# Optimization experiments

Measured on AMD Instinct MI355X. Metric: run time of the kernel, lower is better.

## Reference

```python
import jax, jax.numpy as jnp
import numpy as np

D_MODEL = 1024
D_STATE = 64
HEADDIM = 64
EXPAND = 2
D_INNER = D_MODEL * EXPAND          # 2048
NHEADS = D_INNER // HEADDIM          # 32
D_IN_PROJ = 2 * D_INNER + 2 * D_STATE + NHEADS  # 4256
BATCH, SEQLEN = 4, 4096


def layernorm(x, w, b, eps=1e-5):
    mu = jnp.mean(x, axis=-1, keepdims=True)
    var = jnp.mean(jnp.square(x - mu), axis=-1, keepdims=True)
    return (x - mu) * jax.lax.rsqrt(var + eps) * w + b


def setup_inputs() -> dict:
    key = jax.random.key(0)
    ks = jax.random.split(key, 5)
    x = jax.random.normal(ks[0], (BATCH, SEQLEN, D_MODEL), dtype=jnp.float32)
    # xavier-ish small init (gain 0.5) as in _init_weights
    in_proj_w = jax.random.normal(ks[1], (D_IN_PROJ, D_MODEL), dtype=jnp.float32) * 0.5 * np.sqrt(2.0 / (D_IN_PROJ + D_MODEL))
    out_proj_w = jax.random.normal(ks[2], (D_MODEL, D_INNER), dtype=jnp.float32) * 0.5 * np.sqrt(2.0 / (D_MODEL + D_INNER))
    A_log = jnp.log(jnp.arange(1, NHEADS + 1, dtype=jnp.float32))
    dt_bias = jax.random.normal(ks[3], (NHEADS,), dtype=jnp.float32) * 0.01 + 0.1
    Dparam = jnp.ones((NHEADS,), dtype=jnp.float32)
    return {
        'x': x, 'in_proj_w': in_proj_w, 'out_proj_w': out_proj_w,
        'A_log': A_log, 'dt_bias': dt_bias, 'Dparam': Dparam,
        'ln_w': jnp.ones((D_INNER,), jnp.float32), 'ln_b': jnp.zeros((D_INNER,), jnp.float32),
        'ni_w': jnp.ones((D_MODEL,), jnp.float32), 'ni_b': jnp.zeros((D_MODEL,), jnp.float32),
        'no_w': jnp.ones((D_MODEL,), jnp.float32), 'no_b': jnp.zeros((D_MODEL,), jnp.float32),
    }


def _selective_scan(x_multi, A, Bm, Cm, dt):
    # x_multi: [B,L,H,P], A: [H], Bm/Cm: [B,L,N], dt: [B,L,H]
    Bb, L, H, P = x_multi.shape
    N = Bm.shape[-1]
    dA = jnp.minimum(jnp.exp(dt * A[None, None, :]), 0.99)  # [B,L,H]

    def step(h, inp):
        x_t, B_t, C_t, dA_t = inp  # [B,H,P], [B,N], [B,N], [B,H]
        dBx = jnp.einsum('bhp,bn->bhpn', x_t, B_t)
        h = jnp.clip(dA_t[:, :, None, None] * h + dBx, -10.0, 10.0)
        y_t = jnp.einsum('bn,bhpn->bhp', C_t, h)
        return h, y_t

    h0 = jnp.zeros((Bb, H, P, N), dtype=x_multi.dtype)
    xs = (jnp.moveaxis(x_multi, 1, 0), jnp.moveaxis(Bm, 1, 0),
          jnp.moveaxis(Cm, 1, 0), jnp.moveaxis(dA, 1, 0))
    _, y = jax.lax.scan(step, h0, xs)  # y: [L,B,H,P]
    return jnp.moveaxis(y, 0, 1)


def reference(x, in_proj_w, out_proj_w, A_log, dt_bias, Dparam,
              ln_w, ln_b, ni_w, ni_b, no_w, no_b):
    Bb, L, Dm = x.shape
    x_norm = layernorm(x, ni_w, ni_b)
    zxbcdt = jnp.einsum('bld,ed->ble', x_norm, in_proj_w)  # [B,L,D_IN_PROJ]
    z = zxbcdt[..., :D_INNER]
    x_ssm = zxbcdt[..., D_INNER:2 * D_INNER]
    Bm = zxbcdt[..., 2 * D_INNER:2 * D_INNER + D_STATE]
    Cm = zxbcdt[..., 2 * D_INNER + D_STATE:2 * D_INNER + 2 * D_STATE]
    dt = zxbcdt[..., 2 * D_INNER + 2 * D_STATE:]
    dt = jnp.clip(jax.nn.softplus(dt + dt_bias[None, None, :]), 0.001, 0.1)  # [B,L,H]
    A = -jnp.exp(A_log)  # [H]
    x_multi = x_ssm.reshape(Bb, L, NHEADS, HEADDIM)
    y = _selective_scan(x_multi, A, Bm, Cm, dt)  # [B,L,H,P]
    y = y + x_multi * Dparam[None, None, :, None]  # D skip
    y = y.reshape(Bb, L, D_INNER)
    y = y * jax.nn.silu(z)
    y = layernorm(y, ln_w, ln_b)
    y = jnp.einsum('ble,de->bld', y, out_proj_w)
    y = jnp.clip(y, -10.0, 10.0)
    y = layernorm(y, no_w, no_b)
    return y
```

## Files before the change

kernel.cpp:

```cpp
#include <hip/hip_runtime.h>
#include <hip/hip_bf16.h>
#include <stdint.h>

typedef _Float16 F16;
typedef F16 f16x8 __attribute__((ext_vector_type(8)));
typedef F16 f16x4 __attribute__((ext_vector_type(4)));
typedef float f32x4 __attribute__((ext_vector_type(4)));

#define NTOK   16384
#define DMODEL 1024
#define DINNER 2048
#define DSTATE 64
#define NHEADS 32
#define DINPRJ 4256
#define SEQLEN_ 4096
#define SEGLEN 128
#define NSEG   32

__device__ __forceinline__ void load_lds16(const void* g, void* l) {
  __builtin_amdgcn_global_load_lds((__attribute__((address_space(1))) void*)g,
                                   (__attribute__((address_space(3))) void*)l,
                                   16, 0, 0);
}

__device__ __forceinline__ void lds_st8(F16* base, int row, int col, int rowbytes, f16x8 v) {
  int by = (row * rowbytes + col * 2) ^ ((row & 7) << 4);
  *(f16x8*)((char*)base + by) = v;
}
__device__ __forceinline__ void lds_st1(F16* base, int row, int col, int rowbytes, F16 v) {
  int by = (row * rowbytes + col * 2) ^ ((row & 7) << 4);
  *(F16*)((char*)base + by) = v;
}
__device__ __forceinline__ f16x8 lds_ld8(const F16* base, int row, int col, int rowbytes) {
  int by = (row * rowbytes + col * 2) ^ ((row & 7) << 4);
  return *(const f16x8*)((const char*)base + by);
}

__global__ __launch_bounds__(256) void cvt_kernel(const float* __restrict__ src,
                                                  F16* __restrict__ dst, int n4) {
  int i = blockIdx.x * 256 + threadIdx.x;
  if (i >= n4) return;
  float4 v = *(const float4*)(src + (size_t)i * 4);
  f16x4 o = { (F16)v.x, (F16)v.y, (F16)v.z, (F16)v.w };
  *(f16x4*)(dst + (size_t)i * 4) = o;
}

__device__ __forceinline__ void blk_reduce2(float& s, float& ss) {
  __shared__ float red[8];
#pragma unroll
  for (int m = 32; m >= 1; m >>= 1) { s += __shfl_xor(s, m, 64); ss += __shfl_xor(ss, m, 64); }
  int tid = threadIdx.x, wv = tid >> 6;
  if ((tid & 63) == 0) { red[wv * 2] = s; red[wv * 2 + 1] = ss; }
  __syncthreads();
  s  = red[0] + red[2] + red[4] + red[6];
  ss = red[1] + red[3] + red[5] + red[7];
}

__global__ __launch_bounds__(256) void ln_in_kernel(const float* __restrict__ x,
                                                    const float* __restrict__ w,
                                                    const float* __restrict__ b,
                                                    F16* __restrict__ out) {
  int row = blockIdx.x, tid = threadIdx.x;
  const float* xr = x + (size_t)row * DMODEL + tid * 4;
  float4 v = *(const float4*)xr;
  float s = v.x + v.y + v.z + v.w;
  float ss = v.x * v.x + v.y * v.y + v.z * v.z + v.w * v.w;
  blk_reduce2(s, ss);
  float mu = s * (1.f / DMODEL);
  float var = ss * (1.f / DMODEL) - mu * mu;
  float rs = rsqrtf(var + 1e-5f);
  float4 wv = *(const float4*)(w + tid * 4);
  float4 bv = *(const float4*)(b + tid * 4);
  f16x4 o;
  o.x = (F16)((v.x - mu) * rs * wv.x + bv.x);
  o.y = (F16)((v.y - mu) * rs * wv.y + bv.y);
  o.z = (F16)((v.z - mu) * rs * wv.z + bv.z);
  o.w = (F16)((v.w - mu) * rs * wv.w + bv.w);
  *(f16x4*)(out + (size_t)row * DMODEL + tid * 4) = o;
}

template<int KD, int EPI>
__global__ __launch_bounds__(512, 2)
void gemm_kernel(const F16* __restrict__ A, const F16* __restrict__ W, int Nw,
                 F16* __restrict__ Z, F16* __restrict__ XS,
                 F16* __restrict__ BCH, float* __restrict__ DT,
                 float* __restrict__ O1)
{
  constexpr int NT = KD / 64;
  __shared__ __align__(16) F16 Ab[2][256 * 64];
  __shared__ __align__(16) F16 Bb[2][256 * 64];
  const int tid = threadIdx.x;
  const int lane = tid & 63;
  const int wid = tid >> 6;
  const int wm = wid >> 2, wn = wid & 3;
  const int cpx = gridDim.x >> 3;
  const int id = blockIdx.x;
  const int swz = (id & 7) * cpx + (id >> 3);
  const int m0 = (swz & 63) * 256, n0 = (swz >> 6) * 256;
  const int lr = lane & 15, lk = lane >> 4;

  f32x4 acc[8][4];
#pragma unroll
  for (int i = 0; i < 8; ++i)
#pragma unroll
    for (int j = 0; j < 4; ++j) acc[i][j] = f32x4{0.f, 0.f, 0.f, 0.f};

#define STAGE(T, BUF)                                                          \
  {                                                                            \
    const int k0s = (T) * 64;                                                  \
    _Pragma("unroll")                                                          \
    for (int i = 0; i < 4; ++i) {                                              \
      const int u = i * 512 + tid;                                             \
      const int row = u >> 3;                                                  \
      const int cl = (u & 7) ^ (row & 7);                                      \
      load_lds16(A + (size_t)(m0 + row) * KD + k0s + cl * 8, &Ab[BUF][u * 8]); \
    }                                                                          \
    _Pragma("unroll")                                                          \
    for (int i = 0; i < 4; ++i) {                                              \
      const int u = i * 512 + tid;                                             \
      const int row = u >> 3;                                                  \
      const int cl = (u & 7) ^ (row & 7);                                      \
      int wr = n0 + row; if (wr >= Nw) wr = Nw - 1;                            \
      load_lds16(W + (size_t)wr * KD + k0s + cl * 8, &Bb[BUF][u * 8]);         \
    }                                                                          \
  }

  STAGE(0, 0);
  for (int t = 0; t < NT; ++t) {
    const int cur = t & 1;
    if (t + 1 < NT) {
      STAGE(t + 1, cur ^ 1);
      __builtin_amdgcn_sched_barrier(0);
      asm volatile("s_waitcnt vmcnt(8)" ::: "memory");
    } else {
      __builtin_amdgcn_sched_barrier(0);
      asm volatile("s_waitcnt vmcnt(0)" ::: "memory");
    }
    __builtin_amdgcn_sched_barrier(0);
    __builtin_amdgcn_s_barrier();
    __builtin_amdgcn_sched_barrier(0);

    const F16* Ac = Ab[cur];
    const F16* Bc = Bb[cur];
    f16x8 bfr[4][2];
#pragma unroll
    for (int nf = 0; nf < 4; ++nf)
#pragma unroll
      for (int kk = 0; kk < 2; ++kk)
        bfr[nf][kk] = *(const f16x8*)&Bc[(wn * 64 + nf * 16 + lr) * 64 +
                                         (((kk * 4 + lk) ^ (lr & 7)) * 8)];
#pragma unroll
    for (int mf2 = 0; mf2 < 4; ++mf2) {
      f16x8 af[2][2];
#pragma unroll
      for (int q = 0; q < 2; ++q)
#pragma unroll
        for (int kk = 0; kk < 2; ++kk)
          af[q][kk] = *(const f16x8*)&Ac[(wm * 128 + (mf2 * 2 + q) * 16 + lr) * 64 +
                                         (((kk * 4 + lk) ^ (lr & 7)) * 8)];
#pragma unroll
      for (int q = 0; q < 2; ++q)
#pragma unroll
        for (int nf = 0; nf < 4; ++nf)
#pragma unroll
          for (int kk = 0; kk < 2; ++kk)
            acc[mf2 * 2 + q][nf] = __builtin_amdgcn_mfma_f32_16x16x32_f16(
                af[q][kk], bfr[nf][kk], acc[mf2 * 2 + q][nf], 0, 0, 0);
    }
    __builtin_amdgcn_sched_barrier(0);
    __builtin_amdgcn_s_barrier();
    __builtin_amdgcn_sched_barrier(0);
  }
#undef STAGE

#pragma unroll
  for (int mf = 0; mf < 8; ++mf) {
#pragma unroll
    for (int nf = 0; nf < 4; ++nf) {
      int r0 = m0 + wm * 128 + mf * 16 + lk * 4;
      int c  = n0 + wn * 64 + nf * 16 + lr;
#pragma unroll
      for (int j = 0; j < 4; ++j) {
        float v = acc[mf][nf][j];
        size_t r = (size_t)(r0 + j);
        if (EPI == 1) {
          O1[r * 1024 + c] = v;
        } else {
          if (c < 2048)        Z[r * 2048 + c] = (F16)v;
          else if (c < 4096)   XS[r * 2048 + (c - 2048)] = (F16)v;
          else if (c < 4160)   BCH[r * 128 + (c - 4096)] = (F16)v;
          else if (c < 4224)   BCH[r * 128 + 64 + (c - 4160)] = (F16)v;
          else if (c < 4256)   DT[r * 32 + (c - 4224)] = v;
        }
      }
    }
  }
}

__global__ __launch_bounds__(256) void da_kernel(float* __restrict__ dtraw,
                                                 const float* __restrict__ dt_bias,
                                                 const float* __restrict__ A_log) {
  int idx = blockIdx.x * 256 + threadIdx.x;
  int h = idx & 31;
  float v = dtraw[idx] + dt_bias[h];
  float sp = (v > 20.f) ? v : log1pf(expf(v));
  float dt = fminf(fmaxf(sp, 0.001f), 0.1f);
  float Ah = -expf(A_log[h]);
  dtraw[idx] = fminf(dt * Ah, -0.01005034f);
}

__global__ __launch_bounds__(128) void la_kernel(const float* __restrict__ LD,
                                                 float* __restrict__ LA) {
  const int bh = blockIdx.x, seg = blockIdx.y;
  const int b = bh >> 5, h = bh & 31;
  const int t = threadIdx.x, lane = t & 63;
  size_t tok = (size_t)b * SEQLEN_ + (size_t)seg * SEGLEN + t;
  float v = LD[tok * 32 + h];
#pragma unroll
  for (int m = 1; m <= 32; m <<= 1) {
    float o = __shfl_up(v, m, 64);
    if (lane >= m) v += o;
  }
  __shared__ float w0tot;
  if (t == 63) w0tot = v;
  __syncthreads();
  if (t >= 64) v += w0tot;
  LA[(size_t)bh * SEQLEN_ + (size_t)seg * SEGLEN + t] = v;
}

__global__ __launch_bounds__(256) void ssd_kernel(const F16* __restrict__ BCH,
                                                  const float* __restrict__ LA,
                                                  F16* __restrict__ XS,
                                                  const float* __restrict__ Dparam,
                                                  F16* __restrict__ HLOC) {
  __shared__ __align__(16) F16 Cb[128 * 64];
  __shared__ __align__(16) F16 Bb[128 * 64];
  __shared__ __align__(16) F16 Xb[64 * 128];
  __shared__ __align__(16) F16 Mm[128 * 128];
  const int h = blockIdx.x, seg = blockIdx.y, b = blockIdx.z;
  const int tid = threadIdx.x, lane = tid & 63, w = tid >> 6;
  const int lr = lane & 15, lk = lane >> 4;
  const int bh = b * 32 + h;
  const size_t tok0 = (size_t)b * SEQLEN_ + (size_t)seg * SEGLEN;
  const float* la = LA + (size_t)bh * SEQLEN_ + (size_t)seg * SEGLEN;

  {
    const int t = tid >> 1, half = tid & 1;
    const F16* srcB = BCH + (tok0 + t) * 128 + half * 32;
    const F16* srcC = srcB + 64;
#pragma unroll
    for (int i = 0; i < 4; ++i) {
      lds_st8(Bb, t, half * 32 + i * 8, 128, *(const f16x8*)(srcB + i * 8));
      lds_st8(Cb, t, half * 32 + i * 8, 128, *(const f16x8*)(srcC + i * 8));
    }
  }
#pragma unroll
  for (int pass = 0; pass < 4; ++pass) {
    const int srel = tid & 31, oct = tid >> 5;
    const int s = pass * 32 + srel;
    f16x8 xv = *(const f16x8*)(XS + (tok0 + s) * 2048 + h * 64 + oct * 8);
#pragma unroll
    for (int i = 0; i < 8; ++i)
      lds_st1(Xb, oct * 8 + i, s, 256, xv[i]);
  }
  __syncthreads();

  f32x4 g[2][8];
#pragma unroll
  for (int m = 0; m < 2; ++m)
#pragma unroll
    for (int n = 0; n < 8; ++n) g[m][n] = f32x4{0.f, 0.f, 0.f, 0.f};
#pragma unroll
  for (int kk = 0; kk < 2; ++kk) {
    f16x8 a0 = lds_ld8(Cb, w * 32 + lr,      kk * 32 + lk * 8, 128);
    f16x8 a1 = lds_ld8(Cb, w * 32 + 16 + lr, kk * 32 + lk * 8, 128);
#pragma unroll
    for (int n = 0; n < 8; ++n) {
      f16x8 bq = lds_ld8(Bb, n * 16 + lr, kk * 32 + lk * 8, 128);
      g[0][n] = __builtin_amdgcn_mfma_f32_16x16x32_f16(a0, bq, g[0][n], 0, 0, 0);
      g[1][n] = __builtin_amdgcn_mfma_f32_16x16x32_f16(a1, bq, g[1][n], 0, 0, 0);
    }
  }
  const float Dh = Dparam[h];
  float lat[2][4];
#pragma unroll
  for (int m = 0; m < 2; ++m)
#pragma unroll
    for (int j = 0; j < 4; ++j)
      lat[m][j] = la[w * 32 + m * 16 + lk * 4 + j];
#pragma unroll
  for (int n = 0; n < 8; ++n) {
    const int s = n * 16 + lr;
    const float las = la[s];
#pragma unroll
    for (int m = 0; m < 2; ++m)
#pragma unroll
      for (int j = 0; j < 4; ++j) {
        const int t = w * 32 + m * 16 + lk * 4 + j;
        float v = (s <= t) ? g[m][n][j] * __expf(lat[m][j] - las) : 0.f;
        if (s == t) v += Dh;
        lds_st1(Mm, t, s, 256, (F16)v);
      }
  }
  __syncthreads();

  f32x4 y[2][4];
#pragma unroll
  for (int m = 0; m < 2; ++m)
#pragma unroll
    for (int n = 0; n < 4; ++n) y[m][n] = f32x4{0.f, 0.f, 0.f, 0.f};
#pragma unroll
  for (int kk = 0; kk < 4; ++kk) {
    f16x8 a0 = lds_ld8(Mm, w * 32 + lr,      kk * 32 + lk * 8, 256);
    f16x8 a1 = lds_ld8(Mm, w * 32 + 16 + lr, kk * 32 + lk * 8, 256);
#pragma unroll
    for (int n = 0; n < 4; ++n) {
      f16x8 bq = lds_ld8(Xb, n * 16 + lr, kk * 32 + lk * 8, 256);
      y[0][n] = __builtin_amdgcn_mfma_f32_16x16x32_f16(a0, bq, y[0][n], 0, 0, 0);
      y[1][n] = __builtin_amdgcn_mfma_f32_16x16x32_f16(a1, bq, y[1][n], 0, 0, 0);
    }
  }
#pragma unroll
  for (int m = 0; m < 2; ++m)
#pragma unroll
    for (int n = 0; n < 4; ++n)
#pragma unroll
      for (int j = 0; j < 4; ++j) {
        const int t = w * 32 + m * 16 + lk * 4 + j;
        const int p = n * 16 + lr;
        XS[(tok0 + t) * 2048 + h * 64 + p] = (F16)y[m][n][j];
      }
  __syncthreads();

  {
    const int s = tid >> 1, half = tid & 1;
    const float dec = __expf(la[127] - la[s]);
    const F16* srcB = BCH + (tok0 + s) * 128 + half * 32;
#pragma unroll
    for (int i = 0; i < 4; ++i) {
      f16x8 bv = *(const f16x8*)(srcB + i * 8);
#pragma unroll
      for (int q = 0; q < 8; ++q)
        lds_st1(Mm, half * 32 + i * 8 + q, s, 256, (F16)((float)bv[q] * dec));
    }
  }
  __syncthreads();

  f32x4 hh[4];
#pragma unroll
  for (int n = 0; n < 4; ++n) hh[n] = f32x4{0.f, 0.f, 0.f, 0.f};
#pragma unroll
  for (int kk = 0; kk < 4; ++kk) {
    f16x8 a = lds_ld8(Xb, w * 16 + lr, kk * 32 + lk * 8, 256);
#pragma unroll
    for (int n = 0; n < 4; ++n) {
      f16x8 bq = lds_ld8(Mm, n * 16 + lr, kk * 32 + lk * 8, 256);
      hh[n] = __builtin_amdgcn_mfma_f32_16x16x32_f16(a, bq, hh[n], 0, 0, 0);
    }
  }
  F16* dst = HLOC + ((size_t)bh * NSEG + seg) * 4096;
#pragma unroll
  for (int n = 0; n < 4; ++n)
#pragma unroll
    for (int j = 0; j < 4; ++j) {
      const int p = w * 16 + lk * 4 + j;
      dst[p * 64 + n * 16 + lr] = (F16)hh[n][j];
    }
}

__global__ __launch_bounds__(256) void combine_kernel(F16* __restrict__ HLOC,
                                                      const float* __restrict__ LA) {
  const int bh = blockIdx.x, tid = threadIdx.x;
  const int p = tid >> 2, n0 = (tid & 3) * 16;
  F16* base = HLOC + (size_t)bh * NSEG * 4096 + p * 64 + n0;
  const float* la = LA + (size_t)bh * SEQLEN_;
  union U16 { uint4 v[2]; F16 h[16]; };
  float r[16];
#pragma unroll
  for (int i = 0; i < 16; ++i) r[i] = 0.f;
  for (int k = 0; k < NSEG; ++k) {
    F16* slot = base + (size_t)k * 4096;
    U16 hl; hl.v[0] = *(const uint4*)slot; hl.v[1] = *((const uint4*)slot + 1);
    float P = __expf(la[k * SEGLEN + SEGLEN - 1]);
    U16 ob;
#pragma unroll
    for (int i = 0; i < 16; ++i) ob.h[i] = (F16)r[i];
    *(uint4*)slot = ob.v[0]; *((uint4*)slot + 1) = ob.v[1];
#pragma unroll
    for (int i = 0; i < 16; ++i) r[i] = fmaf(P, r[i], (float)hl.h[i]);
  }
}

__global__ __launch_bounds__(256) void corr_kernel(const F16* __restrict__ BCH,
                                                   const float* __restrict__ LA,
                                                   const F16* __restrict__ HLOC,
                                                   F16* __restrict__ XS) {
  __shared__ __align__(16) F16 Cd[128 * 72];
  __shared__ __align__(16) F16 Hb[64 * 72];
  const int seg = blockIdx.x, h = blockIdx.y, b = blockIdx.z;
  const int tid = threadIdx.x;
  const size_t tok0 = (size_t)b * SEQLEN_ + (size_t)seg * SEGLEN;
  const int bh = b * 32 + h;
  {
    int t = tid >> 1, half = tid & 1;
    float Dv = __expf(LA[(size_t)bh * SEQLEN_ + seg * SEGLEN + t]);
    const F16* src = BCH + (tok0 + t) * 128 + 64 + half * 32;
    F16* dstp = &Cd[t * 72 + half * 32];
#pragma unroll
    for (int i = 0; i < 4; ++i) {
      f16x8 cv = *(const f16x8*)(src + i * 8);
      f16x8 o;
#pragma unroll
      for (int q = 0; q < 8; ++q) o[q] = (F16)(Dv * (float)cv[q]);
      *(f16x8*)(dstp + i * 8) = o;
    }
  }
  {
    int p = tid >> 2, nn = (tid & 3) * 16;
    const F16* src = HLOC + ((size_t)bh * NSEG + seg) * 4096 + p * 64 + nn;
    uint4 a0 = *(const uint4*)src, a1 = *((const uint4*)src + 1);
    *(uint4*)&Hb[p * 72 + nn] = a0;
    *(uint4*)&Hb[p * 72 + nn + 8] = a1;
  }
  __syncthreads();
  const int lane = tid & 63, w = tid >> 6;
  const int lr = lane & 15, lk = lane >> 4;
  f32x4 acc[2][4];
#pragma unroll
  for (int m = 0; m < 2; ++m)
#pragma unroll
    for (int n = 0; n < 4; ++n) acc[m][n] = f32x4{0.f, 0.f, 0.f, 0.f};
#pragma unroll
  for (int kk = 0; kk < 2; ++kk) {
    f16x8 a0 = *(const f16x8*)&Cd[(w * 32 + lr) * 72 + kk * 32 + lk * 8];
    f16x8 a1 = *(const f16x8*)&Cd[(w * 32 + 16 + lr) * 72 + kk * 32 + lk * 8];
#pragma unroll
    for (int n = 0; n < 4; ++n) {
      f16x8 bq = *(const f16x8*)&Hb[(n * 16 + lr) * 72 + kk * 32 + lk * 8];
      acc[0][n] = __builtin_amdgcn_mfma_f32_16x16x32_f16(a0, bq, acc[0][n], 0, 0, 0);
      acc[1][n] = __builtin_amdgcn_mfma_f32_16x16x32_f16(a1, bq, acc[1][n], 0, 0, 0);
    }
  }
#pragma unroll
  for (int m = 0; m < 2; ++m)
#pragma unroll
    for (int n = 0; n < 4; ++n)
#pragma unroll
      for (int j = 0; j < 4; ++j) {
        int t = w * 32 + m * 16 + lk * 4 + j;
        int p = n * 16 + lr;
        F16* yp = XS + (tok0 + t) * 2048 + h * 64 + p;
        *yp = (F16)((float)*yp + acc[m][n][j]);
      }
}

__global__ __launch_bounds__(256) void silu_ln_kernel(F16* __restrict__ Y,
                                                      const F16* __restrict__ Z,
                                                      const float* __restrict__ lnw,
                                                      const float* __restrict__ lnb) {
  int row = blockIdx.x, tid = threadIdx.x;
  size_t base = (size_t)row * DINNER + tid * 8;
  union { uint4 v; F16 h[8]; } yb, zb, ob;
  yb.v = *(const uint4*)(Y + base);
  zb.v = *(const uint4*)(Z + base);
  float vv[8];
  float s = 0.f, ss = 0.f;
#pragma unroll
  for (int i = 0; i < 8; ++i) {
    float y = (float)yb.h[i];
    float z = (float)zb.h[i];
    float sg = 1.f / (1.f + expf(-z));
    float v = y * z * sg;
    vv[i] = v; s += v; ss += v * v;
  }
  blk_reduce2(s, ss);
  float mu = s * (1.f / DINNER);
  float var = ss * (1.f / DINNER) - mu * mu;
  float rs = rsqrtf(var + 1e-5f);
#pragma unroll
  for (int i = 0; i < 8; ++i) {
    float w = lnw[tid * 8 + i], b = lnb[tid * 8 + i];
    ob.h[i] = (F16)((vv[i] - mu) * rs * w + b);
  }
  *(uint4*)(Y + base) = ob.v;
}

__global__ __launch_bounds__(256) void final_ln_kernel(float* __restrict__ O1,
                                                       const float* __restrict__ w,
                                                       const float* __restrict__ b) {
  int row = blockIdx.x, tid = threadIdx.x;
  size_t base = (size_t)row * DMODEL + tid * 4;
  float4 v = *(const float4*)(O1 + base);
  v.x = fminf(fmaxf(v.x, -10.f), 10.f);
  v.y = fminf(fmaxf(v.y, -10.f), 10.f);
  v.z = fminf(fmaxf(v.z, -10.f), 10.f);
  v.w = fminf(fmaxf(v.w, -10.f), 10.f);
  float s = v.x + v.y + v.z + v.w;
  float ss = v.x * v.x + v.y * v.y + v.z * v.z + v.w * v.w;
  blk_reduce2(s, ss);
  float mu = s * (1.f / DMODEL);
  float var = ss * (1.f / DMODEL) - mu * mu;
  float rs = rsqrtf(var + 1e-5f);
  float4 wv = *(const float4*)(w + tid * 4);
  float4 bv = *(const float4*)(b + tid * 4);
  float4 o;
  o.x = (v.x - mu) * rs * wv.x + bv.x;
  o.y = (v.y - mu) * rs * wv.y + bv.y;
  o.z = (v.z - mu) * rs * wv.z + bv.z;
  o.w = (v.w - mu) * rs * wv.w + bv.w;
  *(float4*)(O1 + base) = o;
}

extern "C" void kernel_launch(void* const* d_in, const int* in_sizes, int n_in,
                              void* d_out, int out_size, void* d_ws, size_t ws_size,
                              hipStream_t stream) {
  const float* x       = (const float*)d_in[0];
  const float* w1      = (const float*)d_in[1];
  const float* w2      = (const float*)d_in[2];
  const float* A_log   = (const float*)d_in[3];
  const float* dt_bias = (const float*)d_in[4];
  const float* Dparam  = (const float*)d_in[5];
  const float* ln_w    = (const float*)d_in[6];
  const float* ln_b    = (const float*)d_in[7];
  const float* ni_w    = (const float*)d_in[8];
  const float* ni_b    = (const float*)d_in[9];
  const float* no_w    = (const float*)d_in[10];
  const float* no_b    = (const float*)d_in[11];

  const size_t NEEDED = 119865344ull;
  if (ws_size < NEEDED) return;

  char* wsb = (char*)d_ws;
  F16*   XS   = (F16*)  (wsb + 0ull);
  F16*   BCH  = (F16*)  (wsb + 67108864ull);
  float* DT   = (float*)(wsb + 75497472ull);
  F16*   XN   = (F16*)  (wsb + 77594624ull);
  F16*   W2F  = (F16*)  (wsb + 77594624ull);
  F16*   HLOC = (F16*)  (wsb + 81788928ull);
  float* LA   = (float*)(wsb + 115343360ull);
  F16*   W1F  = (F16*)  (wsb + 111149056ull);

  F16*   Z   = (F16*)d_out;
  float* O1  = (float*)d_out;

  cvt_kernel<<<4256, 256, 0, stream>>>(w1, W1F, (DINPRJ * DMODEL) / 4);
  ln_in_kernel<<<NTOK, 256, 0, stream>>>(x, ni_w, ni_b, XN);
  gemm_kernel<1024, 0><<<64 * 17, 512, 0, stream>>>(
      XN, W1F, DINPRJ, Z, XS, BCH, DT, nullptr);
  cvt_kernel<<<2048, 256, 0, stream>>>(w2, W2F, (DMODEL * DINNER) / 4);
  da_kernel<<<(NTOK * 32) / 256, 256, 0, stream>>>(DT, dt_bias, A_log);
  la_kernel<<<dim3(128, NSEG), 128, 0, stream>>>(DT, LA);
  ssd_kernel<<<dim3(32, NSEG, 4), 256, 0, stream>>>(BCH, LA, XS, Dparam, HLOC);
  combine_kernel<<<128, 256, 0, stream>>>(HLOC, LA);
  corr_kernel<<<dim3(NSEG, 32, 4), 256, 0, stream>>>(BCH, LA, HLOC, XS);
  silu_ln_kernel<<<NTOK, 256, 0, stream>>>(XS, Z, ln_w, ln_b);
  gemm_kernel<2048, 1><<<64 * 4, 512, 0, stream>>>(
      XS, W2F, 1024, nullptr, nullptr, nullptr, nullptr, O1);
  final_ln_kernel<<<NTOK, 256, 0, stream>>>(O1, no_w, no_b);
}
```

Measured before the change: 513.3 us.

## Shrink GEMM tiles to 128x128 with 4 waves and fold dt transform into la_kernel

New measurement: 490.6 us. -4.4%, faster.

```diff
diff --git a/kernel.cpp b/kernel.cpp
--- a/kernel.cpp
+++ b/kernel.cpp
@@ -80,28 +80,28 @@
 }
 
 template<int KD, int EPI>
-__global__ __launch_bounds__(512, 2)
+__global__ __launch_bounds__(256, 2)
 void gemm_kernel(const F16* __restrict__ A, const F16* __restrict__ W, int Nw,
                  F16* __restrict__ Z, F16* __restrict__ XS,
                  F16* __restrict__ BCH, float* __restrict__ DT,
                  float* __restrict__ O1)
 {
   constexpr int NT = KD / 64;
-  __shared__ __align__(16) F16 Ab[2][256 * 64];
-  __shared__ __align__(16) F16 Bb[2][256 * 64];
+  __shared__ __align__(16) F16 Ab[2][128 * 64];
+  __shared__ __align__(16) F16 Bb[2][128 * 64];
   const int tid = threadIdx.x;
   const int lane = tid & 63;
   const int wid = tid >> 6;
-  const int wm = wid >> 2, wn = wid & 3;
-  const int cpx = gridDim.x >> 3;
+  const int wm = wid >> 1, wn = wid & 1;
   const int id = blockIdx.x;
-  const int swz = (id & 7) * cpx + (id >> 3);
-  const int m0 = (swz & 63) * 256, n0 = (swz >> 6) * 256;
+  const int bx = (id & 7) * 16 + ((id >> 3) & 15);
+  const int by = id >> 7;
+  const int m0 = bx * 128, n0 = by * 128;
   const int lr = lane & 15, lk = lane >> 4;
 
-  f32x4 acc[8][4];
-#pragma unroll
-  for (int i = 0; i < 8; ++i)
+  f32x4 acc[4][4];
+#pragma unroll
+  for (int i = 0; i < 4; ++i)
 #pragma unroll
     for (int j = 0; j < 4; ++j) acc[i][j] = f32x4{0.f, 0.f, 0.f, 0.f};
 
@@ -110,14 +110,14 @@
     const int k0s = (T) * 64;                                                  \
     _Pragma("unroll")                                                          \
     for (int i = 0; i < 4; ++i) {                                              \
-      const int u = i * 512 + tid;                                             \
+      const int u = i * 256 + tid;                                             \
       const int row = u >> 3;                                                  \
       const int cl = (u & 7) ^ (row & 7);                                      \
       load_lds16(A + (size_t)(m0 + row) * KD + k0s + cl * 8, &Ab[BUF][u * 8]); \
     }                                                                          \
     _Pragma("unroll")                                                          \
     for (int i = 0; i < 4; ++i) {                                              \
-      const int u = i * 512 + tid;                                             \
+      const int u = i * 256 + tid;                                             \
       const int row = u >> 3;                                                  \
       const int cl = (u & 7) ^ (row & 7);                                      \
       int wr = n0 + row; if (wr >= Nw) wr = Nw - 1;                            \
@@ -142,30 +142,21 @@
 
     const F16* Ac = Ab[cur];
     const F16* Bc = Bb[cur];
-    f16x8 bfr[4][2];
-#pragma unroll
-    for (int nf = 0; nf < 4; ++nf)
-#pragma unroll
-      for (int kk = 0; kk < 2; ++kk)
-        bfr[nf][kk] = *(const f16x8*)&Bc[(wn * 64 + nf * 16 + lr) * 64 +
-                                         (((kk * 4 + lk) ^ (lr & 7)) * 8)];
-#pragma unroll
-    for (int mf2 = 0; mf2 < 4; ++mf2) {
-      f16x8 af[2][2];
-#pragma unroll
-      for (int q = 0; q < 2; ++q)
-#pragma unroll
-        for (int kk = 0; kk < 2; ++kk)
-          af[q][kk] = *(const f16x8*)&Ac[(wm * 128 + (mf2 * 2 + q) * 16 + lr) * 64 +
-                                         (((kk * 4 + lk) ^ (lr & 7)) * 8)];
-#pragma unroll
-      for (int q = 0; q < 2; ++q)
-#pragma unroll
-        for (int nf = 0; nf < 4; ++nf)
-#pragma unroll
-          for (int kk = 0; kk < 2; ++kk)
-            acc[mf2 * 2 + q][nf] = __builtin_amdgcn_mfma_f32_16x16x32_f16(
-                af[q][kk], bfr[nf][kk], acc[mf2 * 2 + q][nf], 0, 0, 0);
+#pragma unroll
+    for (int kk = 0; kk < 2; ++kk) {
+      const int cs = ((kk * 4 + lk) ^ (lr & 7)) * 8;
+      f16x8 af[4], bfr[4];
+#pragma unroll
+      for (int m = 0; m < 4; ++m)
+        af[m] = *(const f16x8*)&Ac[(wm * 64 + m * 16 + lr) * 64 + cs];
+#pragma unroll
+      for (int n = 0; n < 4; ++n)
+        bfr[n] = *(const f16x8*)&Bc[(wn * 64 + n * 16 + lr) * 64 + cs];
+#pragma unroll
+      for (int m = 0; m < 4; ++m)
+#pragma unroll
+        for (int n = 0; n < 4; ++n)
+          acc[m][n] = __builtin_amdgcn_mfma_f32_16x16x32_f16(af[m], bfr[n], acc[m][n], 0, 0, 0);
     }
     __builtin_amdgcn_sched_barrier(0);
     __builtin_amdgcn_s_barrier();
@@ -174,14 +165,14 @@
 #undef STAGE
 
 #pragma unroll
-  for (int mf = 0; mf < 8; ++mf) {
-#pragma unroll
-    for (int nf = 0; nf < 4; ++nf) {
-      int r0 = m0 + wm * 128 + mf * 16 + lk * 4;
-      int c  = n0 + wn * 64 + nf * 16 + lr;
+  for (int m = 0; m < 4; ++m) {
+#pragma unroll
+    for (int n = 0; n < 4; ++n) {
+      int r0 = m0 + wm * 64 + m * 16 + lk * 4;
+      int c  = n0 + wn * 64 + n * 16 + lr;
 #pragma unroll
       for (int j = 0; j < 4; ++j) {
-        float v = acc[mf][nf][j];
+        float v = acc[m][n][j];
         size_t r = (size_t)(r0 + j);
         if (EPI == 1) {
           O1[r * 1024 + c] = v;
@@ -197,25 +188,18 @@
   }
 }
 
-__global__ __launch_bounds__(256) void da_kernel(float* __restrict__ dtraw,
+__global__ __launch_bounds__(128) void la_kernel(const float* __restrict__ DT,
                                                  const float* __restrict__ dt_bias,
-                                                 const float* __restrict__ A_log) {
-  int idx = blockIdx.x * 256 + threadIdx.x;
-  int h = idx & 31;
-  float v = dtraw[idx] + dt_bias[h];
-  float sp = (v > 20.f) ? v : log1pf(expf(v));
-  float dt = fminf(fmaxf(sp, 0.001f), 0.1f);
-  float Ah = -expf(A_log[h]);
-  dtraw[idx] = fminf(dt * Ah, -0.01005034f);
-}
-
-__global__ __launch_bounds__(128) void la_kernel(const float* __restrict__ LD,
+                                                 const float* __restrict__ A_log,
                                                  float* __restrict__ LA) {
   const int bh = blockIdx.x, seg = blockIdx.y;
   const int b = bh >> 5, h = bh & 31;
   const int t = threadIdx.x, lane = t & 63;
   size_t tok = (size_t)b * SEQLEN_ + (size_t)seg * SEGLEN + t;
-  float v = LD[tok * 32 + h];
+  float vraw = DT[tok * 32 + h] + dt_bias[h];
+  float sp = (vraw > 20.f) ? vraw : log1pf(expf(vraw));
+  float dt = fminf(fmaxf(sp, 0.001f), 0.1f);
+  float v = fminf(dt * (-expf(A_log[h])), -0.01005034f);
 #pragma unroll
   for (int m = 1; m <= 32; m <<= 1) {
     float o = __shfl_up(v, m, 64);
@@ -545,16 +529,15 @@
 
   cvt_kernel<<<4256, 256, 0, stream>>>(w1, W1F, (DINPRJ * DMODEL) / 4);
   ln_in_kernel<<<NTOK, 256, 0, stream>>>(x, ni_w, ni_b, XN);
-  gemm_kernel<1024, 0><<<64 * 17, 512, 0, stream>>>(
+  gemm_kernel<1024, 0><<<128 * 34, 256, 0, stream>>>(
       XN, W1F, DINPRJ, Z, XS, BCH, DT, nullptr);
   cvt_kernel<<<2048, 256, 0, stream>>>(w2, W2F, (DMODEL * DINNER) / 4);
-  da_kernel<<<(NTOK * 32) / 256, 256, 0, stream>>>(DT, dt_bias, A_log);
-  la_kernel<<<dim3(128, NSEG), 128, 0, stream>>>(DT, LA);
+  la_kernel<<<dim3(128, NSEG), 128, 0, stream>>>(DT, dt_bias, A_log, LA);
   ssd_kernel<<<dim3(32, NSEG, 4), 256, 0, stream>>>(BCH, LA, XS, Dparam, HLOC);
   combine_kernel<<<128, 256, 0, stream>>>(HLOC, LA);
   corr_kernel<<<dim3(NSEG, 32, 4), 256, 0, stream>>>(BCH, LA, HLOC, XS);
   silu_ln_kernel<<<NTOK, 256, 0, stream>>>(XS, Z, ln_w, ln_b);
-  gemm_kernel<2048, 1><<<64 * 4, 512, 0, stream>>>(
+  gemm_kernel<2048, 1><<<128 * 8, 256, 0, stream>>>(
       XS, W2F, 1024, nullptr, nullptr, nullptr, nullptr, O1);
   final_ln_kernel<<<NTOK, 256, 0, stream>>>(O1, no_w, no_b);
 }
```

## Split GEMM staging into half-tiles interleaved with MFMA phases; fuse dA into scan

Applied to the files above, without the earlier changes.

Result: no change. 518.0 us (+0.9%).

```diff
diff --git a/kernel.cpp b/kernel.cpp
--- a/kernel.cpp
+++ b/kernel.cpp
@@ -87,16 +87,16 @@
                  float* __restrict__ O1)
 {
   constexpr int NT = KD / 64;
-  __shared__ __align__(16) F16 Ab[2][256 * 64];
-  __shared__ __align__(16) F16 Bb[2][256 * 64];
+  __shared__ __align__(16) F16 Ah[2][2][128 * 64];
+  __shared__ __align__(16) F16 Bh[2][2][128 * 64];
   const int tid = threadIdx.x;
   const int lane = tid & 63;
   const int wid = tid >> 6;
   const int wm = wid >> 2, wn = wid & 3;
-  const int cpx = gridDim.x >> 3;
   const int id = blockIdx.x;
-  const int swz = (id & 7) * cpx + (id >> 3);
-  const int m0 = (swz & 63) * 256, n0 = (swz >> 6) * 256;
+  const int bx = (id & 7) * 8 + ((id >> 3) & 7);
+  const int by = id >> 6;
+  const int m0 = bx * 256, n0 = by * 256;
   const int lr = lane & 15, lk = lane >> 4;
 
   f32x4 acc[8][4];
@@ -105,73 +105,79 @@
 #pragma unroll
     for (int j = 0; j < 4; ++j) acc[i][j] = f32x4{0.f, 0.f, 0.f, 0.f};
 
-#define STAGE(T, BUF)                                                          \
-  {                                                                            \
-    const int k0s = (T) * 64;                                                  \
-    _Pragma("unroll")                                                          \
-    for (int i = 0; i < 4; ++i) {                                              \
-      const int u = i * 512 + tid;                                             \
+#define STG_A(T, D, Q)                                                         \
+  { _Pragma("unroll")                                                          \
+    for (int ps = 0; ps < 2; ++ps) {                                           \
+      const int u = ps * 512 + tid;                                            \
       const int row = u >> 3;                                                  \
       const int cl = (u & 7) ^ (row & 7);                                      \
-      load_lds16(A + (size_t)(m0 + row) * KD + k0s + cl * 8, &Ab[BUF][u * 8]); \
-    }                                                                          \
-    _Pragma("unroll")                                                          \
-    for (int i = 0; i < 4; ++i) {                                              \
-      const int u = i * 512 + tid;                                             \
+      load_lds16(A + (size_t)(m0 + (Q) * 128 + row) * KD + (T) * 64 + cl * 8,  \
+                 &Ah[D][Q][u * 8]);                                            \
+    } }
+#define STG_B(T, D, Q)                                                         \
+  { _Pragma("unroll")                                                          \
+    for (int ps = 0; ps < 2; ++ps) {                                           \
+      const int u = ps * 512 + tid;                                            \
       const int row = u >> 3;                                                  \
       const int cl = (u & 7) ^ (row & 7);                                      \
-      int wr = n0 + row; if (wr >= Nw) wr = Nw - 1;                            \
-      load_lds16(W + (size_t)wr * KD + k0s + cl * 8, &Bb[BUF][u * 8]);         \
+      int wr = n0 + (Q) * 128 + row; if (wr >= Nw) wr = Nw - 1;                \
+      load_lds16(W + (size_t)wr * KD + (T) * 64 + cl * 8, &Bh[D][Q][u * 8]);   \
+    } }
+
+#define PHASE(MF0)                                                             \
+  { f16x8 af0[2], af1[2];                                                      \
+    _Pragma("unroll")                                                          \
+    for (int kk = 0; kk < 2; ++kk) {                                           \
+      const int cs = ((kk * 4 + lk) ^ (lr & 7)) * 8;                           \
+      af0[kk] = *(const f16x8*)&Ac[((MF0) * 16 + lr) * 64 + cs];               \
+      af1[kk] = *(const f16x8*)&Ac[((MF0) * 16 + 16 + lr) * 64 + cs];          \
     }                                                                          \
-  }
-
-  STAGE(0, 0);
+    __builtin_amdgcn_s_setprio(1);                                             \
+    _Pragma("unroll")                                                          \
+    for (int nf = 0; nf < 4; ++nf)                                             \
+      _Pragma("unroll")                                                        \
+      for (int kk = 0; kk < 2; ++kk) {                                         \
+        acc[(MF0)][nf] = __builtin_amdgcn_mfma_f32_16x16x32_f16(               \
+            af0[kk], bfr[nf][kk], acc[(MF0)][nf], 0, 0, 0);                    \
+        acc[(MF0) + 1][nf] = __builtin_amdgcn_mfma_f32_16x16x32_f16(           \
+            af1[kk], bfr[nf][kk], acc[(MF0) + 1][nf], 0, 0, 0);                \
+      }                                                                        \
+    __builtin_amdgcn_s_setprio(0); }
+
+  STG_A(0, 0, 0); STG_A(0, 0, 1); STG_B(0, 0, 0); STG_B(0, 0, 1);
   for (int t = 0; t < NT; ++t) {
-    const int cur = t & 1;
-    if (t + 1 < NT) {
-      STAGE(t + 1, cur ^ 1);
-      __builtin_amdgcn_sched_barrier(0);
-      asm volatile("s_waitcnt vmcnt(8)" ::: "memory");
-    } else {
-      __builtin_amdgcn_sched_barrier(0);
-      asm volatile("s_waitcnt vmcnt(0)" ::: "memory");
-    }
+    const int d = t & 1;
+    const bool more = (t + 1 < NT);
+    if (more) { STG_A(t + 1, d ^ 1, 0); STG_A(t + 1, d ^ 1, 1); }
+    if (more) { asm volatile("s_waitcnt vmcnt(4)" ::: "memory"); }
+    else      { asm volatile("s_waitcnt vmcnt(0)" ::: "memory"); }
     __builtin_amdgcn_sched_barrier(0);
     __builtin_amdgcn_s_barrier();
     __builtin_amdgcn_sched_barrier(0);
 
-    const F16* Ac = Ab[cur];
-    const F16* Bc = Bb[cur];
+    const F16* Ac = Ah[d][wm];
+    const F16* Bc = Bh[d][wn >> 1];
+    const int br0 = (wn & 1) * 64;
     f16x8 bfr[4][2];
 #pragma unroll
     for (int nf = 0; nf < 4; ++nf)
 #pragma unroll
       for (int kk = 0; kk < 2; ++kk)
-        bfr[nf][kk] = *(const f16x8*)&Bc[(wn * 64 + nf * 16 + lr) * 64 +
+        bfr[nf][kk] = *(const f16x8*)&Bc[(br0 + nf * 16 + lr) * 64 +
                                          (((kk * 4 + lk) ^ (lr & 7)) * 8)];
-#pragma unroll
-    for (int mf2 = 0; mf2 < 4; ++mf2) {
-      f16x8 af[2][2];
-#pragma unroll
-      for (int q = 0; q < 2; ++q)
-#pragma unroll
-        for (int kk = 0; kk < 2; ++kk)
-          af[q][kk] = *(const f16x8*)&Ac[(wm * 128 + (mf2 * 2 + q) * 16 + lr) * 64 +
-                                         (((kk * 4 + lk) ^ (lr & 7)) * 8)];
-#pragma unroll
-      for (int q = 0; q < 2; ++q)
-#pragma unroll
-        for (int nf = 0; nf < 4; ++nf)
-#pragma unroll
-          for (int kk = 0; kk < 2; ++kk)
-            acc[mf2 * 2 + q][nf] = __builtin_amdgcn_mfma_f32_16x16x32_f16(
-                af[q][kk], bfr[nf][kk], acc[mf2 * 2 + q][nf], 0, 0, 0);
-    }
+    PHASE(0);
+    if (more) STG_B(t + 1, d ^ 1, 0);
+    PHASE(2);
+    if (more) STG_B(t + 1, d ^ 1, 1);
+    PHASE(4);
+    PHASE(6);
     __builtin_amdgcn_sched_barrier(0);
     __builtin_amdgcn_s_barrier();
     __builtin_amdgcn_sched_barrier(0);
   }
-#undef STAGE
+#undef STG_A
+#undef STG_B
+#undef PHASE
 
 #pragma unroll
   for (int mf = 0; mf < 8; ++mf) {
@@ -197,25 +203,18 @@
   }
 }
 
-__global__ __launch_bounds__(256) void da_kernel(float* __restrict__ dtraw,
+__global__ __launch_bounds__(128) void la_kernel(const float* __restrict__ DT,
                                                  const float* __restrict__ dt_bias,
-                                                 const float* __restrict__ A_log) {
-  int idx = blockIdx.x * 256 + threadIdx.x;
-  int h = idx & 31;
-  float v = dtraw[idx] + dt_bias[h];
-  float sp = (v > 20.f) ? v : log1pf(expf(v));
-  float dt = fminf(fmaxf(sp, 0.001f), 0.1f);
-  float Ah = -expf(A_log[h]);
-  dtraw[idx] = fminf(dt * Ah, -0.01005034f);
-}
-
-__global__ __launch_bounds__(128) void la_kernel(const float* __restrict__ LD,
+                                                 const float* __restrict__ A_log,
                                                  float* __restrict__ LA) {
   const int bh = blockIdx.x, seg = blockIdx.y;
   const int b = bh >> 5, h = bh & 31;
   const int t = threadIdx.x, lane = t & 63;
   size_t tok = (size_t)b * SEQLEN_ + (size_t)seg * SEGLEN + t;
-  float v = LD[tok * 32 + h];
+  float vraw = DT[tok * 32 + h] + dt_bias[h];
+  float sp = (vraw > 20.f) ? vraw : log1pf(expf(vraw));
+  float dt = fminf(fmaxf(sp, 0.001f), 0.1f);
+  float v = fminf(dt * (-expf(A_log[h])), -0.01005034f);
 #pragma unroll
   for (int m = 1; m <= 32; m <<= 1) {
     float o = __shfl_up(v, m, 64);
@@ -548,8 +547,7 @@
   gemm_kernel<1024, 0><<<64 * 17, 512, 0, stream>>>(
       XN, W1F, DINPRJ, Z, XS, BCH, DT, nullptr);
   cvt_kernel<<<2048, 256, 0, stream>>>(w2, W2F, (DMODEL * DINNER) / 4);
-  da_kernel<<<(NTOK * 32) / 256, 256, 0, stream>>>(DT, dt_bias, A_log);
-  la_kernel<<<dim3(128, NSEG), 128, 0, stream>>>(DT, LA);
+  la_kernel<<<dim3(128, NSEG), 128, 0, stream>>>(DT, dt_bias, A_log, LA);
   ssd_kernel<<<dim3(32, NSEG, 4), 256, 0, stream>>>(BCH, LA, XS, Dparam, HLOC);
   combine_kernel<<<128, 256, 0, stream>>>(HLOC, LA);
   corr_kernel<<<dim3(NSEG, 32, 4), 256, 0, stream>>>(BCH, LA, HLOC, XS);
```

## Pipeline GEMM with quarter-tile LDS ring, interleaved loads, and fuse dA into scan

Applied to the files above, without the earlier changes.

Result: faster. 497.9 us (-3.0%).

```diff
diff --git a/kernel.cpp b/kernel.cpp
--- a/kernel.cpp
+++ b/kernel.cpp
@@ -35,6 +35,13 @@
   int by = (row * rowbytes + col * 2) ^ ((row & 7) << 4);
   return *(const f16x8*)((const char*)base + by);
 }
+
+#define SBAR()                                                                 \
+  {                                                                            \
+    __builtin_amdgcn_sched_barrier(0);                                         \
+    __builtin_amdgcn_s_barrier();                                              \
+    __builtin_amdgcn_sched_barrier(0);                                         \
+  }
 
 __global__ __launch_bounds__(256) void cvt_kernel(const float* __restrict__ src,
                                                   F16* __restrict__ dst, int n4) {
@@ -87,16 +94,16 @@
                  float* __restrict__ O1)
 {
   constexpr int NT = KD / 64;
-  __shared__ __align__(16) F16 Ab[2][256 * 64];
-  __shared__ __align__(16) F16 Bb[2][256 * 64];
+  __shared__ __align__(16) F16 As[4 * 128 * 64];
+  __shared__ __align__(16) F16 Bs[4 * 128 * 64];
   const int tid = threadIdx.x;
   const int lane = tid & 63;
   const int wid = tid >> 6;
   const int wm = wid >> 2, wn = wid & 3;
-  const int cpx = gridDim.x >> 3;
   const int id = blockIdx.x;
-  const int swz = (id & 7) * cpx + (id >> 3);
-  const int m0 = (swz & 63) * 256, n0 = (swz >> 6) * 256;
+  const int bx = (id & 7) * 8 + ((id >> 3) & 7);
+  const int by = id >> 6;
+  const int m0 = bx * 256, n0 = by * 256;
   const int lr = lane & 15, lk = lane >> 4;
 
   f32x4 acc[8][4];
@@ -105,73 +112,80 @@
 #pragma unroll
     for (int j = 0; j < 4; ++j) acc[i][j] = f32x4{0.f, 0.f, 0.f, 0.f};
 
-#define STAGE(T, BUF)                                                          \
-  {                                                                            \
-    const int k0s = (T) * 64;                                                  \
+#define STG_HALF(POS)                                                          \
+  if ((POS) < 4 * NT) {                                                        \
+    const int tl = (POS) >> 2, hh = (POS) & 3;                                 \
+    const int hb = hh & 1;                                                     \
+    F16* dsts = ((hh < 2) ? Bs : As) + (((2 * tl + hb) & 3) * (128 * 64));     \
+    const int k0s = tl * 64;                                                   \
     _Pragma("unroll")                                                          \
-    for (int i = 0; i < 4; ++i) {                                              \
+    for (int i = 0; i < 2; ++i) {                                              \
       const int u = i * 512 + tid;                                             \
       const int row = u >> 3;                                                  \
       const int cl = (u & 7) ^ (row & 7);                                      \
-      load_lds16(A + (size_t)(m0 + row) * KD + k0s + cl * 8, &Ab[BUF][u * 8]); \
+      if (hh < 2) {                                                            \
+        int wr = n0 + hb * 128 + row; if (wr >= Nw) wr = Nw - 1;               \
+        load_lds16(W + (size_t)wr * KD + k0s + cl * 8, dsts + u * 8);          \
+      } else {                                                                 \
+        load_lds16(A + (size_t)(m0 + hb * 128 + row) * KD + k0s + cl * 8,      \
+                   dsts + u * 8);                                              \
+      }                                                                        \
     }                                                                          \
-    _Pragma("unroll")                                                          \
-    for (int i = 0; i < 4; ++i) {                                              \
-      const int u = i * 512 + tid;                                             \
-      const int row = u >> 3;                                                  \
-      const int cl = (u & 7) ^ (row & 7);                                      \
-      int wr = n0 + row; if (wr >= Nw) wr = Nw - 1;                            \
-      load_lds16(W + (size_t)wr * KD + k0s + cl * 8, &Bb[BUF][u * 8]);         \
-    }                                                                          \
-  }
-
-  STAGE(0, 0);
-  for (int t = 0; t < NT; ++t) {
-    const int cur = t & 1;
-    if (t + 1 < NT) {
-      STAGE(t + 1, cur ^ 1);
+  }
+
+  STG_HALF(0); STG_HALF(1); STG_HALF(2); STG_HALF(3); STG_HALF(4); STG_HALF(5);
+  __builtin_amdgcn_sched_barrier(0);
+  asm volatile("s_waitcnt vmcnt(4)" ::: "memory");
+  SBAR();
+
+  for (int j = 0; j < NT; ++j) {
+    const F16* Aslot = As + (((2 * j + wm) & 3) * (128 * 64));
+    const F16* Bslot = Bs + (((2 * j + (wn >> 1)) & 3) * (128 * 64));
+    f16x8 bfr[4][2];
+#pragma unroll
+    for (int q = 0; q < 4; ++q) {
+      if (q == 0) {
+#pragma unroll
+        for (int nf = 0; nf < 4; ++nf)
+#pragma unroll
+          for (int kk = 0; kk < 2; ++kk)
+            bfr[nf][kk] = *(const f16x8*)&Bslot[((wn & 1) * 64 + nf * 16 + lr) * 64 +
+                                                (((kk * 4 + lk) ^ (lr & 7)) * 8)];
+      }
+      f16x8 af0[2], af1[2];
+#pragma unroll
+      for (int kk = 0; kk < 2; ++kk) {
+        const int cs = ((kk * 4 + lk) ^ (lr & 7)) * 8;
+        af0[kk] = *(const f16x8*)&Aslot[((2 * q) * 16 + lr) * 64 + cs];
+        af1[kk] = *(const f16x8*)&Aslot[((2 * q + 1) * 16 + lr) * 64 + cs];
+      }
+      STG_HALF(4 * j + 6 + q);
+      SBAR();
+      asm volatile("s_waitcnt lgkmcnt(0)" ::: "memory");
       __builtin_amdgcn_sched_barrier(0);
-      asm volatile("s_waitcnt vmcnt(8)" ::: "memory");
-    } else {
-      __builtin_amdgcn_sched_barrier(0);
-      asm volatile("s_waitcnt vmcnt(0)" ::: "memory");
-    }
-    __builtin_amdgcn_sched_barrier(0);
-    __builtin_amdgcn_s_barrier();
-    __builtin_amdgcn_sched_barrier(0);
-
-    const F16* Ac = Ab[cur];
-    const F16* Bc = Bb[cur];
-    f16x8 bfr[4][2];
-#pragma unroll
-    for (int nf = 0; nf < 4; ++nf)
-#pragma unroll
-      for (int kk = 0; kk < 2; ++kk)
-        bfr[nf][kk] = *(const f16x8*)&Bc[(wn * 64 + nf * 16 + lr) * 64 +
-                                         (((kk * 4 + lk) ^ (lr & 7)) * 8)];
-#pragma unroll
-    for (int mf2 = 0; mf2 < 4; ++mf2) {
-      f16x8 af[2][2];
-#pragma unroll
-      for (int q = 0; q < 2; ++q)
-#pragma unroll
-        for (int kk = 0; kk < 2; ++kk)
-          af[q][kk] = *(const f16x8*)&Ac[(wm * 128 + (mf2 * 2 + q) * 16 + lr) * 64 +
-                                         (((kk * 4 + lk) ^ (lr & 7)) * 8)];
-#pragma unroll
-      for (int q = 0; q < 2; ++q)
-#pragma unroll
-        for (int nf = 0; nf < 4; ++nf)
-#pragma unroll
-          for (int kk = 0; kk < 2; ++kk)
-            acc[mf2 * 2 + q][nf] = __builtin_amdgcn_mfma_f32_16x16x32_f16(
-                af[q][kk], bfr[nf][kk], acc[mf2 * 2 + q][nf], 0, 0, 0);
-    }
-    __builtin_amdgcn_sched_barrier(0);
-    __builtin_amdgcn_s_barrier();
-    __builtin_amdgcn_sched_barrier(0);
-  }
-#undef STAGE
+      __builtin_amdgcn_s_setprio(1);
+#pragma unroll
+      for (int nf = 0; nf < 4; ++nf)
+#pragma unroll
+        for (int kk = 0; kk < 2; ++kk) {
+          acc[2 * q][nf] = __builtin_amdgcn_mfma_f32_16x16x32_f16(
+              af0[kk], bfr[nf][kk], acc[2 * q][nf], 0, 0, 0);
+          acc[2 * q + 1][nf] = __builtin_amdgcn_mfma_f32_16x16x32_f16(
+              af1[kk], bfr[nf][kk], acc[2 * q + 1][nf], 0, 0, 0);
+        }
+      __builtin_amdgcn_s_setprio(0);
+      if (q == 3) {
+        __builtin_amdgcn_sched_barrier(0);
+        if (j + 2 < NT) {
+          asm volatile("s_waitcnt vmcnt(4)" ::: "memory");
+        } else if (j + 2 == NT) {
+          asm volatile("s_waitcnt vmcnt(0)" ::: "memory");
+        }
+      }
+      SBAR();
+    }
+  }
+#undef STG_HALF
 
 #pragma unroll
   for (int mf = 0; mf < 8; ++mf) {
@@ -197,25 +211,18 @@
   }
 }
 
-__global__ __launch_bounds__(256) void da_kernel(float* __restrict__ dtraw,
+__global__ __launch_bounds__(128) void la_kernel(const float* __restrict__ DT,
                                                  const float* __restrict__ dt_bias,
-                                                 const float* __restrict__ A_log) {
-  int idx = blockIdx.x * 256 + threadIdx.x;
-  int h = idx & 31;
-  float v = dtraw[idx] + dt_bias[h];
-  float sp = (v > 20.f) ? v : log1pf(expf(v));
-  float dt = fminf(fmaxf(sp, 0.001f), 0.1f);
-  float Ah = -expf(A_log[h]);
-  dtraw[idx] = fminf(dt * Ah, -0.01005034f);
-}
-
-__global__ __launch_bounds__(128) void la_kernel(const float* __restrict__ LD,
+                                                 const float* __restrict__ A_log,
                                                  float* __restrict__ LA) {
   const int bh = blockIdx.x, seg = blockIdx.y;
   const int b = bh >> 5, h = bh & 31;
   const int t = threadIdx.x, lane = t & 63;
   size_t tok = (size_t)b * SEQLEN_ + (size_t)seg * SEGLEN + t;
-  float v = LD[tok * 32 + h];
+  float vraw = DT[tok * 32 + h] + dt_bias[h];
+  float sp = (vraw > 20.f) ? vraw : log1pf(expf(vraw));
+  float dt = fminf(fmaxf(sp, 0.001f), 0.1f);
+  float v = fminf(dt * (-expf(A_log[h])), -0.01005034f);
 #pragma unroll
   for (int m = 1; m <= 32; m <<= 1) {
     float o = __shfl_up(v, m, 64);
@@ -548,8 +555,7 @@
   gemm_kernel<1024, 0><<<64 * 17, 512, 0, stream>>>(
       XN, W1F, DINPRJ, Z, XS, BCH, DT, nullptr);
   cvt_kernel<<<2048, 256, 0, stream>>>(w2, W2F, (DMODEL * DINNER) / 4);
-  da_kernel<<<(NTOK * 32) / 256, 256, 0, stream>>>(DT, dt_bias, A_log);
-  la_kernel<<<dim3(128, NSEG), 128, 0, stream>>>(DT, LA);
+  la_kernel<<<dim3(128, NSEG), 128, 0, stream>>>(DT, dt_bias, A_log, LA);
   ssd_kernel<<<dim3(32, NSEG, 4), 256, 0, stream>>>(BCH, LA, XS, Dparam, HLOC);
   combine_kernel<<<128, 256, 0, stream>>>(HLOC, LA);
   corr_kernel<<<dim3(NSEG, 32, 4), 256, 0, stream>>>(BCH, LA, HLOC, XS);
```
